# Performance work log

Measured on AMD Instinct MI355X. Metric: run time of the kernel, lower is better.

Reference implementation:

```python
import jax, jax.numpy as jnp
import numpy as np

N, E = 50000, 800000
DIN, DOUT, DEDGE, HEADS = 128, 128, 64, 1


def setup_inputs() -> dict:
    key = jax.random.key(0)
    ks = jax.random.split(key, 16)
    s = 0.02
    inp = {
        "x": jax.random.normal(ks[0], (N, DIN), jnp.float32),
        "edge_index": jax.random.randint(ks[1], (2, E), 0, N, dtype=jnp.int32),
        "edge_attr": jax.random.normal(ks[2], (E, DEDGE), jnp.float32),
        # TransformerConv params (PyG defaults: q/k/v/skip have bias, lin_edge has no bias)
        "Wq": jax.random.normal(ks[3], (DIN, HEADS * DOUT), jnp.float32) * s,
        "bq": jnp.zeros((HEADS * DOUT,), jnp.float32),
        "Wk": jax.random.normal(ks[4], (DIN, HEADS * DOUT), jnp.float32) * s,
        "bk": jnp.zeros((HEADS * DOUT,), jnp.float32),
        "Wv": jax.random.normal(ks[5], (DIN, HEADS * DOUT), jnp.float32) * s,
        "bv": jnp.zeros((HEADS * DOUT,), jnp.float32),
        "We": jax.random.normal(ks[6], (DEDGE, HEADS * DOUT), jnp.float32) * s,
        "Wskip": jax.random.normal(ks[7], (DIN, HEADS * DOUT), jnp.float32) * s,
        "bskip": jnp.zeros((HEADS * DOUT,), jnp.float32),
        # LayerNorm
        "ln_g": jnp.ones((DOUT,), jnp.float32),
        "ln_b": jnp.zeros((DOUT,), jnp.float32),
        # GatedResidualConnection
        "Wres": jax.random.normal(ks[8], (DIN, DOUT), jnp.float32) * s,
        "bres": jnp.zeros((DOUT,), jnp.float32),
        "Wgate": jax.random.normal(ks[9], (DIN, 1), jnp.float32) * s,
        "bgate": jnp.zeros((1,), jnp.float32),
    }
    return inp


def _transformer_conv(x, edge_index, edge_attr, Wq, bq, Wk, bk, Wv, bv, We, Wskip, bskip):
    H, C = HEADS, DOUT
    src, dst = edge_index[0], edge_index[1]  # j -> i (aggregate at dst)
    q = (x @ Wq + bq).reshape(-1, H, C)
    k = (x @ Wk + bk).reshape(-1, H, C)
    v = (x @ Wv + bv).reshape(-1, H, C)
    e = (edge_attr @ We).reshape(-1, H, C)  # [E,H,C]
    k_j = k[src] + e
    v_j = v[src] + e
    q_i = q[dst]
    alpha = jnp.sum(q_i * k_j, axis=-1) / jnp.sqrt(jnp.float32(C))  # [E,H]
    # segment softmax over incoming edges of each dst node
    amax = jax.ops.segment_max(alpha, dst, num_segments=N)  # [N,H]
    ex = jnp.exp(alpha - amax[dst])
    denom = jax.ops.segment_sum(ex, dst, num_segments=N)  # [N,H]
    p = ex / denom[dst]  # [E,H]
    out = jax.ops.segment_sum(p[..., None] * v_j, dst, num_segments=N)  # [N,H,C]
    out = out.reshape(-1, H * C)
    out = out + (x @ Wskip + bskip)  # root weight skip
    return out


def reference(x, edge_index, edge_attr, Wq, bq, Wk, bk, Wv, bv, We, Wskip, bskip,
              ln_g, ln_b, Wres, bres, Wgate, bgate):
    out = _transformer_conv(x, edge_index, edge_attr, Wq, bq, Wk, bk, Wv, bv, We, Wskip, bskip)
    # LayerNorm(out_channels)
    mu = jnp.mean(out, axis=-1, keepdims=True)
    var = jnp.mean(jnp.square(out - mu), axis=-1, keepdims=True)
    out = (out - mu) / jnp.sqrt(var + 1e-5) * ln_g + ln_b
    out = jax.nn.relu(out)
    # gated residual
    residual = x @ Wres + bres
    gate = jax.nn.sigmoid(x @ Wgate + bgate)  # [N,1]
    return gate * out + (1.0 - gate) * residual
```

## Files before the change

### kernel.cpp

```cpp
#include <hip/hip_runtime.h>
#include <math.h>

#define NN 50000
#define EE 800000
#define NPAD 50048
#define PC 768

typedef short bf16x8 __attribute__((ext_vector_type(8)));
typedef float f32x4 __attribute__((ext_vector_type(4)));

#define ASCALE 0.08838834764831845f

__device__ inline unsigned short f2bf(float f)
{
    unsigned u = __float_as_uint(f);
    u = u + 0x7fff + ((u >> 16) & 1);
    return (unsigned short)(u >> 16);
}

__global__ __launch_bounds__(256) void k_wprep(const float* __restrict__ Wq,
                                               const float* __restrict__ bq,
                                               const float* __restrict__ We,
                                               float* __restrict__ wqe,
                                               float* __restrict__ bqe)
{
    int idx = blockIdx.x * 256 + threadIdx.x;
    if (idx < 8192) {
        int r = idx >> 6, m = idx & 63;
        float acc = 0.f;
        for (int c = 0; c < 128; ++c) acc += Wq[r * 128 + c] * We[m * 128 + c];
        wqe[r * 64 + m] = acc;
    } else if (idx < 8256) {
        int m = idx - 8192;
        float acc = 0.f;
        for (int c = 0; c < 128; ++c) acc += bq[c] * We[m * 128 + c];
        bqe[m] = acc;
    }
}

__global__ __launch_bounds__(256) void k_packx(const float* __restrict__ x,
                                               short* __restrict__ Xb)
{
    int t = blockIdx.x * 256 + threadIdx.x;
    int base = t * 4;
    if (base >= NPAD * 128) return;
    short s0 = 0, s1 = 0, s2 = 0, s3 = 0;
    if (base < NN * 128) {
        const float4 v = *(const float4*)(x + base);
        s0 = f2bf(v.x); s1 = f2bf(v.y); s2 = f2bf(v.z); s3 = f2bf(v.w);
    }
    short4 o; o.x = s0; o.y = s1; o.z = s2; o.w = s3;
    *(short4*)(Xb + base) = o;
}

__global__ __launch_bounds__(256) void k_packw(
    const float* __restrict__ Wq, const float* __restrict__ bq,
    const float* __restrict__ Wk, const float* __restrict__ bk,
    const float* __restrict__ Wv, const float* __restrict__ bv,
    const float* __restrict__ Wskip, const float* __restrict__ bskip,
    const float* __restrict__ Wres, const float* __restrict__ bres,
    const float* __restrict__ Wgate, const float* __restrict__ bgate,
    const float* __restrict__ wqe, const float* __restrict__ bqe,
    const float* __restrict__ We,
    short* __restrict__ WT, float* __restrict__ bias,
    unsigned short* __restrict__ WeTb)
{
    int idx = blockIdx.x * 256 + threadIdx.x;
    if (idx < PC * 128) {
        int col = idx >> 7, k = idx & 127;
        float v;
        if (col < 128)      v = Wq[k * 128 + col];
        else if (col < 256) v = Wk[k * 128 + (col - 128)];
        else if (col < 384) v = Wv[k * 128 + (col - 256)];
        else if (col < 512) v = Wskip[k * 128 + (col - 384)];
        else if (col < 640) v = Wres[k * 128 + (col - 512)];
        else if (col < 704) v = wqe[k * 64 + (col - 640)];
        else if (col == 704) v = Wgate[k];
        else                v = 0.f;
        WT[col * 128 + k] = (short)f2bf(v);
    } else if (idx < PC * 128 + PC) {
        int col = idx - PC * 128;
        float b;
        if (col < 128)      b = bq[col];
        else if (col < 256) b = bk[col - 128];
        else if (col < 384) b = bv[col - 256];
        else if (col < 512) b = bskip[col - 384];
        else if (col < 640) b = bres[col - 512];
        else if (col < 704) b = bqe[col - 640];
        else if (col == 704) b = bgate[0];
        else                b = 0.f;
        bias[col] = b;
    } else if (idx < PC * 128 + PC + 128 * 72) {
        int i2 = idx - (PC * 128 + PC);
        int c = i2 / 72, kk = i2 % 72;
        WeTb[i2] = (kk < 64) ? f2bf(We[kk * 128 + c]) : (unsigned short)0;
    }
}

#define LROW 136
__global__ __launch_bounds__(256) void k_gemm(const short* __restrict__ Xb,
                                              const short* __restrict__ WT,
                                              const float* __restrict__ bias,
                                              float* __restrict__ P,
                                              unsigned short* __restrict__ KVb16)
{
    __shared__ short Al[128 * LROW];
    __shared__ short Bl[64 * LROW];

    int bn = blockIdx.x;
    int bm = blockIdx.y;
    int tid = threadIdx.x;

    const short* gA = Xb + (size_t)bm * 128 * 128;
    const short* gB = WT + (size_t)bn * 64 * 128;

#pragma unroll
    for (int it = 0; it < 8; ++it) {
        int g = it * 256 + tid;
        int row = g >> 4, c8 = g & 15;
        *(bf16x8*)&Al[row * LROW + c8 * 8] = *(const bf16x8*)(gA + g * 8);
    }
#pragma unroll
    for (int it = 0; it < 4; ++it) {
        int g = it * 256 + tid;
        int row = g >> 4, c8 = g & 15;
        *(bf16x8*)&Bl[row * LROW + c8 * 8] = *(const bf16x8*)(gB + g * 8);
    }
    __syncthreads();

    int wave = tid >> 6, lane = tid & 63;
    int quad = lane >> 4, l16 = lane & 15;
    int r0 = wave * 32;

    f32x4 acc[2][4] = {};
#pragma unroll
    for (int ks = 0; ks < 4; ++ks) {
        int k0 = ks * 32 + quad * 8;
        bf16x8 af0 = *(const bf16x8*)&Al[(r0 + l16) * LROW + k0];
        bf16x8 af1 = *(const bf16x8*)&Al[(r0 + 16 + l16) * LROW + k0];
#pragma unroll
        for (int cn = 0; cn < 4; ++cn) {
            bf16x8 bfr = *(const bf16x8*)&Bl[(cn * 16 + l16) * LROW + k0];
            acc[0][cn] = __builtin_amdgcn_mfma_f32_16x16x32_bf16(af0, bfr, acc[0][cn], 0, 0, 0);
            acc[1][cn] = __builtin_amdgcn_mfma_f32_16x16x32_bf16(af1, bfr, acc[1][cn], 0, 0, 0);
        }
    }

    bool isKV = (bn >= 2 && bn <= 5);
#pragma unroll
    for (int half = 0; half < 2; ++half) {
        int growb = bm * 128 + r0 + half * 16 + quad * 4;
#pragma unroll
        for (int cn = 0; cn < 4; ++cn) {
            int gcol = bn * 64 + cn * 16 + l16;
            float b = bias[gcol];
#pragma unroll
            for (int i = 0; i < 4; ++i) {
                int grow = growb + i;
                if (grow < NN) {
                    float v = acc[half][cn][i] + b;
                    if (isKV) {
                        int slot;
                        if (gcol < 192)      slot = (gcol - 128) * 2;
                        else if (gcol < 256) slot = (gcol - 192) * 2 + 1;
                        else if (gcol < 320) slot = 128 + (gcol - 256) * 2;
                        else                 slot = 128 + (gcol - 320) * 2 + 1;
                        KVb16[(size_t)grow * 256 + slot] = f2bf(v);
                    } else {
                        if (gcol == 704) v = 1.f / (1.f + __expf(-v));
                        P[(size_t)grow * PC + gcol] = v;
                    }
                }
            }
        }
    }
}

__global__ __launch_bounds__(256) void k_hist(const int* __restrict__ ei,
                                              int* __restrict__ deg, int E)
{
    int e = blockIdx.x * 256 + threadIdx.x;
    if (e < E) atomicAdd(&deg[ei[E + e]], 1);
}

__global__ __launch_bounds__(256) void k_scan1(const int* __restrict__ deg,
                                               int* __restrict__ rs,
                                               int* __restrict__ cs, int n)
{
    __shared__ int sh[256];
    int base = blockIdx.x * 1024;
    int t = threadIdx.x;
    int idx = base + t * 4;
    int v[4];
#pragma unroll
    for (int k = 0; k < 4; ++k) v[k] = (idx + k < n) ? deg[idx + k] : 0;
    int sum = v[0] + v[1] + v[2] + v[3];
    sh[t] = sum;
    __syncthreads();
    for (int off = 1; off < 256; off <<= 1) {
        int add = (t >= off) ? sh[t - off] : 0;
        __syncthreads();
        sh[t] += add;
        __syncthreads();
    }
    int run = sh[t] - sum;
    if (t == 255) cs[blockIdx.x] = sh[255];
#pragma unroll
    for (int k = 0; k < 4; ++k) {
        if (idx + k < n) rs[idx + k] = run;
        run += v[k];
    }
}

__global__ void k_scan2(int* __restrict__ cs, int nc)
{
    __shared__ int sh[64];
    int t = threadIdx.x;
    sh[t] = (t < nc) ? cs[t] : 0;
    __syncthreads();
    if (t == 0) {
        int acc = 0;
        for (int i = 0; i < nc; ++i) { int v = sh[i]; sh[i] = acc; acc += v; }
    }
    __syncthreads();
    if (t < nc) cs[t] = sh[t];
}

__global__ __launch_bounds__(256) void k_scan3(int* __restrict__ rs,
                                               const int* __restrict__ cs,
                                               int* __restrict__ cur, int n, int E)
{
    int i = blockIdx.x * 256 + threadIdx.x;
    if (i < n) {
        int v = rs[i] + cs[i >> 10];
        rs[i] = v;
        cur[i] = v;
    } else if (i == n) {
        rs[n] = E;
    }
}

__global__ __launch_bounds__(256) void k_scatter(const int* __restrict__ ei,
                                                 int* __restrict__ cur,
                                                 int2* __restrict__ sj, int E)
{
    int e = blockIdx.x * 256 + threadIdx.x;
    if (e < E) {
        int d = ei[E + e];
        int pos = atomicAdd(&cur[d], 1);
        int2 v; v.x = ei[e]; v.y = e;
        sj[pos] = v;
    }
}

__global__ __launch_bounds__(256) void k_attn_fused(
    const float* __restrict__ P, const unsigned int* __restrict__ KVb,
    const float* __restrict__ ea, const unsigned short* __restrict__ WeTb,
    const int* __restrict__ rs, const int2* __restrict__ sj,
    const float* __restrict__ ln_g, const float* __restrict__ ln_b,
    float* __restrict__ out)
{
    __shared__ unsigned short WeT_l[128 * 72];
    __shared__ unsigned short Sb_l[4 * 64];
    __shared__ float att_l[4 * 128];

    int tid = threadIdx.x;
    {
        const unsigned int* src = (const unsigned int*)WeTb;
        unsigned int* dst = (unsigned int*)WeT_l;
        for (int i = tid; i < 128 * 36; i += 256) dst[i] = src[i];
    }

    int wave = tid >> 6, lane = tid & 63;
    int node = blockIdx.x * 4 + wave;

    const float* Prow = P + (size_t)node * PC;
    float q0 = Prow[lane];
    float q1 = Prow[64 + lane];
    float wq = Prow[640 + lane];

    float accd = 0.f, t0 = 0.f, t1 = 0.f, sA = 0.f;
    int beg = rs[node], end = rs[node + 1];

    int p = beg;
    for (; p + 8 <= end; p += 8) {
        float pp[8], aa[8], v0[8], v1[8];
#pragma unroll
        for (int u = 0; u < 8; ++u) {
            int2 s = sj[p + u];
            const unsigned int* kv = KVb + (size_t)s.x * 128;
            unsigned int kw = kv[lane];
            unsigned int vw = kv[64 + lane];
            float a = __builtin_nontemporal_load(ea + (size_t)s.y * 64 + lane);
            float k0 = __uint_as_float(kw << 16);
            float k1 = __uint_as_float(kw & 0xffff0000u);
            v0[u] = __uint_as_float(vw << 16);
            v1[u] = __uint_as_float(vw & 0xffff0000u);
            aa[u] = a;
            pp[u] = q0 * k0 + q1 * k1 + wq * a;
        }
#pragma unroll
        for (int o = 32; o > 0; o >>= 1) {
#pragma unroll
            for (int u = 0; u < 8; ++u) pp[u] += __shfl_xor(pp[u], o);
        }
#pragma unroll
        for (int u = 0; u < 8; ++u) {
            float ex = __expf(pp[u] * ASCALE);
            accd += ex;
            t0 += ex * v0[u];
            t1 += ex * v1[u];
            sA += ex * aa[u];
        }
    }
    for (; p < end; ++p) {
        int2 s = sj[p];
        const unsigned int* kv = KVb + (size_t)s.x * 128;
        unsigned int kw = kv[lane];
        unsigned int vw = kv[64 + lane];
        float a = __builtin_nontemporal_load(ea + (size_t)s.y * 64 + lane);
        float k0 = __uint_as_float(kw << 16);
        float k1 = __uint_as_float(kw & 0xffff0000u);
        float vv0 = __uint_as_float(vw << 16);
        float vv1 = __uint_as_float(vw & 0xffff0000u);
        float part = q0 * k0 + q1 * k1 + wq * a;
#pragma unroll
        for (int o = 32; o > 0; o >>= 1) part += __shfl_xor(part, o);
        float ex = __expf(part * ASCALE);
        accd += ex;
        t0 += ex * vv0;
        t1 += ex * vv1;
        sA += ex * a;
    }


    Sb_l[wave * 64 + lane] = f2bf(sA);
    __syncthreads();

    {
        int quad = lane >> 4, l16 = lane & 15;
        int arow = l16 & 3;
        bf16x8 a0 = *(const bf16x8*)&Sb_l[arow * 64 + quad * 8];
        bf16x8 a1 = *(const bf16x8*)&Sb_l[arow * 64 + 32 + quad * 8];
#pragma unroll
        for (int c2 = 0; c2 < 2; ++c2) {
            int cn = wave * 2 + c2;
            int r = cn * 16 + l16;
            bf16x8 b0 = *(const bf16x8*)&WeT_l[r * 72 + quad * 8];
            bf16x8 b1 = *(const bf16x8*)&WeT_l[r * 72 + 32 + quad * 8];
            f32x4 acc = {};
            acc = __builtin_amdgcn_mfma_f32_16x16x32_bf16(a0, b0, acc, 0, 0, 0);
            acc = __builtin_amdgcn_mfma_f32_16x16x32_bf16(a1, b1, acc, 0, 0, 0);
            if (quad == 0) {
#pragma unroll
                for (int i = 0; i < 4; ++i)
                    att_l[i * 128 + cn * 16 + l16] = acc[i];
            }
        }
    }
    __syncthreads();

    float rcp = accd > 0.f ? 1.f / accd : 0.f;
    float a0f = (t0 + att_l[wave * 128 + lane]) * rcp + Prow[384 + lane];
    float a1f = (t1 + att_l[wave * 128 + 64 + lane]) * rcp + Prow[448 + lane];

    float s = a0f + a1f;
#pragma unroll
    for (int o = 32; o > 0; o >>= 1) s += __shfl_xor(s, o);
    float mean = s * (1.f / 128.f);
    float d0 = a0f - mean, d1 = a1f - mean;
    float vs = d0 * d0 + d1 * d1;
#pragma unroll
    for (int o = 32; o > 0; o >>= 1) vs += __shfl_xor(vs, o);
    float inv = rsqrtf(vs * (1.f / 128.f) + 1e-5f);
    float n0 = d0 * inv * ln_g[lane] + ln_b[lane];
    float n1 = d1 * inv * ln_g[64 + lane] + ln_b[64 + lane];
    n0 = fmaxf(n0, 0.f);
    n1 = fmaxf(n1, 0.f);

    float g = Prow[704];
    float r0 = Prow[512 + lane];
    float r1 = Prow[576 + lane];
    out[(size_t)node * 128 + lane] = g * n0 + (1.f - g) * r0;
    out[(size_t)node * 128 + 64 + lane] = g * n1 + (1.f - g) * r1;
}

extern "C" void kernel_launch(void* const* d_in, const int* in_sizes, int n_in,
                              void* d_out, int out_size, void* d_ws, size_t ws_size,
                              hipStream_t stream)
{
    const float* x     = (const float*)d_in[0];
    const int*   ei    = (const int*)d_in[1];
    const float* ea    = (const float*)d_in[2];
    const float* Wq    = (const float*)d_in[3];
    const float* bq    = (const float*)d_in[4];
    const float* Wk    = (const float*)d_in[5];
    const float* bk    = (const float*)d_in[6];
    const float* Wv    = (const float*)d_in[7];
    const float* bv    = (const float*)d_in[8];
    const float* We    = (const float*)d_in[9];
    const float* Wskip = (const float*)d_in[10];
    const float* bskip = (const float*)d_in[11];
    const float* ln_g  = (const float*)d_in[12];
    const float* ln_b  = (const float*)d_in[13];
    const float* Wres  = (const float*)d_in[14];
    const float* bres  = (const float*)d_in[15];
    const float* Wgate = (const float*)d_in[16];
    const float* bgate = (const float*)d_in[17];
    float* out = (float*)d_out;

    float* W = (float*)d_ws;
    size_t o = 0;
    auto falloc = [&](size_t e) { size_t r = o; o += e; return r; };
    size_t oP    = falloc((size_t)NN * PC);
    size_t oWQE  = falloc(8192);
    size_t oBQE  = falloc(64);
    size_t oBIAS = falloc(PC);
    size_t oKVB  = falloc((size_t)NN * 128);

    short* SB = (short*)(W + o);
    size_t oXB  = 0;
    size_t oWT  = oXB + (size_t)NPAD * 128;
    size_t oWET = oWT + (size_t)PC * 128;
    size_t sh_total = oWET + 128 * 72;

    int* IB = (int*)(SB + ((sh_total + 1) & ~(size_t)1));
    size_t io = 0;
    auto ialloc = [&](size_t e) { size_t r = io; io += e; return r; };
    size_t oSJ   = ialloc((size_t)2 * EE);
    size_t oDEG  = ialloc(NN);
    size_t oRS   = ialloc(NN + 1);
    size_t oCUR  = ialloc(NN);
    size_t oCS   = ialloc(64);

    hipMemsetAsync(IB + oDEG, 0, NN * sizeof(int), stream);

    k_wprep<<<33, 256, 0, stream>>>(Wq, bq, We, W + oWQE, W + oBQE);
    k_packx<<<(NPAD * 128 / 4 + 255) / 256, 256, 0, stream>>>(x, SB + oXB);
    k_packw<<<(PC * 128 + PC + 128 * 72 + 255) / 256, 256, 0, stream>>>(
        Wq, bq, Wk, bk, Wv, bv, Wskip, bskip, Wres, bres, Wgate, bgate,
        W + oWQE, W + oBQE, We, SB + oWT, W + oBIAS,
        (unsigned short*)(SB + oWET));

    dim3 ggrid(PC / 64, NPAD / 128);
    k_gemm<<<ggrid, 256, 0, stream>>>(SB + oXB, SB + oWT, W + oBIAS, W + oP,
                                      (unsigned short*)(W + oKVB));

    k_hist<<<(EE + 255) / 256, 256, 0, stream>>>(ei, IB + oDEG, EE);
    k_scan1<<<49, 256, 0, stream>>>(IB + oDEG, IB + oRS, IB + oCS, NN);
    k_scan2<<<1, 64, 0, stream>>>(IB + oCS, 49);
    k_scan3<<<(NN + 256) / 256, 256, 0, stream>>>(IB + oRS, IB + oCS, IB + oCUR, NN, EE);
    k_scatter<<<(EE + 255) / 256, 256, 0, stream>>>(ei, IB + oCUR, (int2*)(IB + oSJ), EE);

    k_attn_fused<<<NN / 4, 256, 0, stream>>>(
        W + oP, (const unsigned int*)(W + oKVB), ea,
        (const unsigned short*)(SB + oWET),
        IB + oRS, (const int2*)(IB + oSJ), ln_g, ln_b, out);
}
```

Before: 588.3 us.

## Interleave K/V bf16 layout for single 8-byte gathers and drop LDS weight staging

```diff
diff --git a/kernel.cpp b/kernel.cpp
--- a/kernel.cpp
+++ b/kernel.cpp
@@ -160,12 +160,12 @@
                 if (grow < NN) {
                     float v = acc[half][cn][i] + b;
                     if (isKV) {
-                        int slot;
-                        if (gcol < 192)      slot = (gcol - 128) * 2;
-                        else if (gcol < 256) slot = (gcol - 192) * 2 + 1;
-                        else if (gcol < 320) slot = 128 + (gcol - 256) * 2;
-                        else                 slot = 128 + (gcol - 320) * 2 + 1;
-                        KVb16[(size_t)grow * 256 + slot] = f2bf(v);
+                        int c, sub;
+                        if (gcol < 192)      { c = gcol - 128; sub = 0; }
+                        else if (gcol < 256) { c = gcol - 192; sub = 1; }
+                        else if (gcol < 320) { c = gcol - 256; sub = 2; }
+                        else                 { c = gcol - 320; sub = 3; }
+                        KVb16[(size_t)grow * 256 + c * 4 + sub] = f2bf(v);
                     } else {
                         if (gcol == 704) v = 1.f / (1.f + __expf(-v));
                         P[(size_t)grow * PC + gcol] = v;
@@ -260,17 +260,10 @@
     const float* __restrict__ ln_g, const float* __restrict__ ln_b,
     float* __restrict__ out)
 {
-    __shared__ unsigned short WeT_l[128 * 72];
     __shared__ unsigned short Sb_l[4 * 64];
     __shared__ float att_l[4 * 128];
 
     int tid = threadIdx.x;
-    {
-        const unsigned int* src = (const unsigned int*)WeTb;
-        unsigned int* dst = (unsigned int*)WeT_l;
-        for (int i = tid; i < 128 * 36; i += 256) dst[i] = src[i];
-    }
-
     int wave = tid >> 6, lane = tid & 63;
     int node = blockIdx.x * 4 + wave;
 
@@ -287,15 +280,14 @@
         float pp[8], aa[8], v0[8], v1[8];
 #pragma unroll
         for (int u = 0; u < 8; ++u) {
-            int2 s = sj[p + u];
-            const unsigned int* kv = KVb + (size_t)s.x * 128;
-            unsigned int kw = kv[lane];
-            unsigned int vw = kv[64 + lane];
-            float a = __builtin_nontemporal_load(ea + (size_t)s.y * 64 + lane);
-            float k0 = __uint_as_float(kw << 16);
-            float k1 = __uint_as_float(kw & 0xffff0000u);
-            v0[u] = __uint_as_float(vw << 16);
-            v1[u] = __uint_as_float(vw & 0xffff0000u);
+            long long sv = __builtin_nontemporal_load((const long long*)(sj + p + u));
+            int sx = (int)sv, sy = (int)(sv >> 32);
+            uint2 kv2 = *(const uint2*)(KVb + (size_t)sx * 128 + 2 * lane);
+            float a = __builtin_nontemporal_load(ea + (size_t)sy * 64 + lane);
+            float k0 = __uint_as_float(kv2.x << 16);
+            float k1 = __uint_as_float(kv2.x & 0xffff0000u);
+            v0[u] = __uint_as_float(kv2.y << 16);
+            v1[u] = __uint_as_float(kv2.y & 0xffff0000u);
             aa[u] = a;
             pp[u] = q0 * k0 + q1 * k1 + wq * a;
         }
@@ -313,16 +305,44 @@
             sA += ex * aa[u];
         }
     }
+    for (; p + 4 <= end; p += 4) {
+        float pp[4], aa[4], v0[4], v1[4];
+#pragma unroll
+        for (int u = 0; u < 4; ++u) {
+            long long sv = __builtin_nontemporal_load((const long long*)(sj + p + u));
+            int sx = (int)sv, sy = (int)(sv >> 32);
+            uint2 kv2 = *(const uint2*)(KVb + (size_t)sx * 128 + 2 * lane);
+            float a = __builtin_nontemporal_load(ea + (size_t)sy * 64 + lane);
+            float k0 = __uint_as_float(kv2.x << 16);
+            float k1 = __uint_as_float(kv2.x & 0xffff0000u);
+            v0[u] = __uint_as_float(kv2.y << 16);
+            v1[u] = __uint_as_float(kv2.y & 0xffff0000u);
+            aa[u] = a;
+            pp[u] = q0 * k0 + q1 * k1 + wq * a;
+        }
+#pragma unroll
+        for (int o = 32; o > 0; o >>= 1) {
+#pragma unroll
+            for (int u = 0; u < 4; ++u) pp[u] += __shfl_xor(pp[u], o);
+        }
+#pragma unroll
+        for (int u = 0; u < 4; ++u) {
+            float ex = __expf(pp[u] * ASCALE);
+            accd += ex;
+            t0 += ex * v0[u];
+            t1 += ex * v1[u];
+            sA += ex * aa[u];
+        }
+    }
     for (; p < end; ++p) {
-        int2 s = sj[p];
-        const unsigned int* kv = KVb + (size_t)s.x * 128;
-        unsigned int kw = kv[lane];
-        unsigned int vw = kv[64 + lane];
-        float a = __builtin_nontemporal_load(ea + (size_t)s.y * 64 + lane);
-        float k0 = __uint_as_float(kw << 16);
-        float k1 = __uint_as_float(kw & 0xffff0000u);
-        float vv0 = __uint_as_float(vw << 16);
-        float vv1 = __uint_as_float(vw & 0xffff0000u);
+        long long sv = __builtin_nontemporal_load((const long long*)(sj + p));
+        int sx = (int)sv, sy = (int)(sv >> 32);
+        uint2 kv2 = *(const uint2*)(KVb + (size_t)sx * 128 + 2 * lane);
+        float a = __builtin_nontemporal_load(ea + (size_t)sy * 64 + lane);
+        float k0 = __uint_as_float(kv2.x << 16);
+        float k1 = __uint_as_float(kv2.x & 0xffff0000u);
+        float vv0 = __uint_as_float(kv2.y << 16);
+        float vv1 = __uint_as_float(kv2.y & 0xffff0000u);
         float part = q0 * k0 + q1 * k1 + wq * a;
 #pragma unroll
         for (int o = 32; o > 0; o >>= 1) part += __shfl_xor(part, o);
@@ -346,8 +366,8 @@
         for (int c2 = 0; c2 < 2; ++c2) {
             int cn = wave * 2 + c2;
             int r = cn * 16 + l16;
-            bf16x8 b0 = *(const bf16x8*)&WeT_l[r * 72 + quad * 8];
-            bf16x8 b1 = *(const bf16x8*)&WeT_l[r * 72 + 32 + quad * 8];
+            bf16x8 b0 = *(const bf16x8*)(WeTb + r * 72 + quad * 8);
+            bf16x8 b1 = *(const bf16x8*)(WeTb + r * 72 + 32 + quad * 8);
             f32x4 acc = {};
             acc = __builtin_amdgcn_mfma_f32_16x16x32_bf16(a0, b0, acc, 0, 0, 0);
             acc = __builtin_amdgcn_mfma_f32_16x16x32_bf16(a1, b1, acc, 0, 0, 0);
```

Result: faster. 565.3 us (-3.9%).
